# Kernel optimization log

Hardware: AMD Instinct MI355X
Metric: run time of the kernel (lower is better)

The kernel has to match this reference:

```python
import jax, jax.numpy as jnp
import numpy as np
import math

EPS = 1.1920929e-07  # torch.finfo(float32).eps, used by nn.RMSNorm when eps=None
N_HEADS = 16

def _rmsnorm(x, w):
    return x * jax.lax.rsqrt(jnp.mean(x * x, axis=-1, keepdims=True) + EPS) * w

def setup_inputs() -> dict:
    key = jax.random.key(0)
    D, V, FF = 1024, 32000, 2048
    NS, IPS = 4, 8
    B, T = 2, 1024
    ks = jax.random.split(key, 8)
    sd = 0.02
    g = lambda i, shape: jax.random.normal(ks[i], shape, jnp.float32) * sd
    return {
        "tokens": jax.random.randint(ks[0], (B, T), 0, V),
        "embed_w": g(1, (V, D)),
        "qkv_w": g(2, (3 * D, D)),
        "o_w": g(3, (D, D)),
        "gate_w": g(4, (FF, D)),
        "up_w": g(5, (FF, D)),
        "down_w": g(6, (D, FF)),
        "norm1_w": jnp.ones((D,), jnp.float32),
        "norm2_w": jnp.ones((D,), jnp.float32),
        "scale_gamma": jnp.ones((NS, D), jnp.float32),
        "scale_beta": jnp.zeros((NS, D), jnp.float32),
        "iter_scale": jnp.ones((NS, IPS), jnp.float32),
        "norm_w": jnp.ones((D,), jnp.float32),
        "lm_head_w": g(7, (V, D)),
    }

def _block(x, gamma, beta, qkv_w, o_w, gate_w, up_w, down_w, norm1_w, norm2_w):
    B, T, D = x.shape
    hd = D // N_HEADS
    # pre-attn norm + FiLM modulation
    h = _rmsnorm(x, norm1_w) * gamma + beta
    qkv = (h @ qkv_w.T).reshape(B, T, 3, N_HEADS, hd)
    q = jnp.transpose(qkv[:, :, 0], (0, 2, 1, 3))  # [B,H,T,hd]
    k = jnp.transpose(qkv[:, :, 1], (0, 2, 1, 3))
    v = jnp.transpose(qkv[:, :, 2], (0, 2, 1, 3))
    scores = jnp.einsum('bhqd,bhkd->bhqk', q, k) / math.sqrt(hd)
    causal = jnp.tril(jnp.ones((T, T), dtype=bool))
    scores = jnp.where(causal, scores, -jnp.inf)
    attn = jax.nn.softmax(scores, axis=-1)
    out = jnp.einsum('bhqk,bhkd->bhqd', attn, v)
    out = jnp.transpose(out, (0, 2, 1, 3)).reshape(B, T, D)
    x = x + out @ o_w.T
    # pre-FFN norm + FiLM modulation, SwiGLU
    h2 = _rmsnorm(x, norm2_w) * gamma + beta
    x = x + (jax.nn.silu(h2 @ gate_w.T) * (h2 @ up_w.T)) @ down_w.T
    return x

def reference(tokens, embed_w, qkv_w, o_w, gate_w, up_w, down_w, norm1_w,
              norm2_w, scale_gamma, scale_beta, iter_scale, norm_w, lm_head_w):
    NS, IPS = iter_scale.shape
    x = embed_w[tokens].astype(jnp.float32)  # [B,T,D]
    # flatten (scale, iter) schedule to per-virtual-layer params [NS*IPS, ...]
    gammas = jnp.repeat(scale_gamma, IPS, axis=0)
    betas = jnp.repeat(scale_beta, IPS, axis=0)
    iters = iter_scale.reshape(-1)

    @jax.checkpoint
    def step(x, per):
        g, b, s = per
        y = _block(x, g, b, qkv_w, o_w, gate_w, up_w, down_w, norm1_w, norm2_w)
        return x + (y - x) * s, None

    x, _ = jax.lax.scan(step, x, (gammas, betas, iters))
    return _rmsnorm(x, norm_w) @ lm_head_w.T  # [B,T,V]
```

## Files before the change

kernel.cpp:

```cpp
#include <hip/hip_runtime.h>

typedef __bf16 bf16;
typedef __attribute__((ext_vector_type(8))) __bf16 bf16x8;
typedef __attribute__((ext_vector_type(4))) __bf16 bf16x4;
typedef __attribute__((ext_vector_type(4))) float f32x4;

#define MFMA16(a,b,c) __builtin_amdgcn_mfma_f32_16x16x32_bf16((a),(b),(c),0,0,0)

__device__ __forceinline__ void gload16(const void* g, void* l) {
    __builtin_amdgcn_global_load_lds((const __attribute__((address_space(1))) void*)g,
                                     (__attribute__((address_space(3))) void*)l, 16, 0, 0);
}

__device__ __forceinline__ int xcd_swizzle(int orig, int nwg) {
    int q = nwg >> 3, r = nwg & 7;
    int xcd = orig & 7, loc = orig >> 3;
    int base = (xcd < r) ? xcd * (q + 1) : r * (q + 1) + (xcd - r) * q;
    return base + loc;
}


__global__ __launch_bounds__(256) void cvt_kernel(const float* __restrict__ in,
                                                  bf16* __restrict__ out, int n4) {
    int stride = gridDim.x * 256;
    for (int i = blockIdx.x * 256 + threadIdx.x; i < n4; i += stride) {
        float4 v = ((const float4*)in)[i];
        bf16x4 o;
        o[0] = (bf16)v.x; o[1] = (bf16)v.y; o[2] = (bf16)v.z; o[3] = (bf16)v.w;
        ((bf16x4*)out)[i] = o;
    }
}

__global__ __launch_bounds__(256) void embed_kernel(const int* __restrict__ tok,
                                                    const float* __restrict__ ew,
                                                    float* __restrict__ X) {
    int m = blockIdx.x;
    int t = tok[m];
    ((float4*)(X + (size_t)m * 1024))[threadIdx.x] =
        ((const float4*)(ew + (size_t)t * 1024))[threadIdx.x];
}

template <bool FILM>
__global__ __launch_bounds__(256) void rmsnorm_kernel(const float* __restrict__ X,
                                                      const float* __restrict__ w,
                                                      const float* __restrict__ gamma,
                                                      const float* __restrict__ beta,
                                                      bf16* __restrict__ H) {
    int m = blockIdx.x, t = threadIdx.x;
    float4 xv = ((const float4*)(X + (size_t)m * 1024))[t];
    float ss = xv.x * xv.x + xv.y * xv.y + xv.z * xv.z + xv.w * xv.w;
#pragma unroll
    for (int off = 1; off < 64; off <<= 1) ss += __shfl_xor(ss, off);
    __shared__ float red[4];
    if ((t & 63) == 0) red[t >> 6] = ss;
    __syncthreads();
    float tot = red[0] + red[1] + red[2] + red[3];
    float sc = rsqrtf(tot * (1.0f / 1024.0f) + 1.1920929e-07f);
    float4 wv = ((const float4*)w)[t];
    float r0 = xv.x * sc * wv.x, r1 = xv.y * sc * wv.y;
    float r2 = xv.z * sc * wv.z, r3 = xv.w * sc * wv.w;
    if (FILM) {
        float4 gv = ((const float4*)gamma)[t];
        float4 bv = ((const float4*)beta)[t];
        r0 = r0 * gv.x + bv.x; r1 = r1 * gv.y + bv.y;
        r2 = r2 * gv.z + bv.z; r3 = r3 * gv.w + bv.w;
    }
    bf16x4 o;
    o[0] = (bf16)r0; o[1] = (bf16)r1; o[2] = (bf16)r2; o[3] = (bf16)r3;
    ((bf16x4*)(H + (size_t)m * 1024))[t] = o;
}


template <int MT, int MODE, bool BNF>
__device__ __forceinline__ void gemm_body(const bf16* __restrict__ A,
                                          const bf16* __restrict__ B,
                                          int GN, int GM, int N, int K,
                                          bf16* __restrict__ Cb, float* __restrict__ Cf,
                                          const float* __restrict__ Xin,
                                          const float* __restrict__ Xin2,
                                          float* __restrict__ Xout,
                                          const float* __restrict__ sptr,
                                          bf16* __restrict__ VTp) {
    constexpr int BM = 32 * MT;
    __shared__ __align__(16) bf16 As[BM * 64];
    __shared__ __align__(16) bf16 Bs[128 * 64];
    const int wg = xcd_swizzle(blockIdx.x, GN * GM);
    int bn, bm;
    if (BNF) { bm = wg / GN; bn = wg - bm * GN; }
    else     { bn = wg / GM; bm = wg - bn * GM; }
    const int tid = threadIdx.x, lane = tid & 63, w = tid >> 6;
    const int wr = w >> 1, wc = w & 1, lr = lane & 15, lg = lane >> 4;
    const bf16* Ab = A + (size_t)bm * BM * K;
    const bf16* Bb = B + (size_t)bn * 128 * K;

    f32x4 acc[MT][4];
#pragma unroll
    for (int i = 0; i < MT; ++i)
#pragma unroll
        for (int j = 0; j < 4; ++j) acc[i][j] = (f32x4){0.f, 0.f, 0.f, 0.f};

    for (int kt = 0; kt < K; kt += 64) {
        __syncthreads();
#pragma unroll
        for (int i = 0; i < MT; ++i) {
            int cw = i * 256 + w * 64;
            int cid = cw + lane;
            gload16(Ab + (size_t)(cid >> 3) * K + kt + (cid & 7) * 8, As + cw * 8);
        }
#pragma unroll
        for (int i = 0; i < 4; ++i) {
            int cw = i * 256 + w * 64;
            int cid = cw + lane;
            gload16(Bb + (size_t)(cid >> 3) * K + kt + (cid & 7) * 8, Bs + cw * 8);
        }
        __syncthreads();
#pragma unroll
        for (int kk = 0; kk < 64; kk += 32) {
            bf16x8 af[MT], bfr[4];
#pragma unroll
            for (int mi = 0; mi < MT; ++mi)
                af[mi] = *(const bf16x8*)(As + (wr * (16 * MT) + mi * 16 + lr) * 64 + kk + lg * 8);
#pragma unroll
            for (int ni = 0; ni < 4; ++ni)
                bfr[ni] = *(const bf16x8*)(Bs + (wc * 64 + ni * 16 + lr) * 64 + kk + lg * 8);
#pragma unroll
            for (int mi = 0; mi < MT; ++mi)
#pragma unroll
                for (int ni = 0; ni < 4; ++ni)
                    acc[mi][ni] = MFMA16(af[mi], bfr[ni], acc[mi][ni]);
        }
    }

    float s1 = (MODE == 2) ? sptr[0] : 0.f;
    if (MODE == 4 && bn >= 16) {
#pragma unroll
        for (int mi = 0; mi < MT; ++mi) {
#pragma unroll
            for (int ni = 0; ni < 4; ++ni) {
                int row0 = bm * BM + wr * (16 * MT) + mi * 16 + lg * 4;
                int col = bn * 128 + wc * 64 + ni * 16 + lr;
                int h = (col - 2048) >> 6, d = (col - 2048) & 63;
                int bb = row0 >> 10, t0 = row0 & 1023;
                bf16x4 pv;
#pragma unroll
                for (int j = 0; j < 4; ++j) pv[j] = (bf16)acc[mi][ni][j];
                *(bf16x4*)(VTp + (size_t)(bb * 16 + h) * 65536 + (size_t)d * 1024 + t0) = pv;
            }
        }
        return;
    }
#pragma unroll
    for (int mi = 0; mi < MT; ++mi) {
#pragma unroll
        for (int ni = 0; ni < 4; ++ni) {
#pragma unroll
            for (int j = 0; j < 4; ++j) {
                int row = bm * BM + wr * (16 * MT) + mi * 16 + lg * 4 + j;
                int col = bn * 128 + wc * 64 + ni * 16 + lr;
                size_t idx = (size_t)row * N + col;
                float v = acc[mi][ni][j];
                if (MODE == 0 || MODE == 4) Cb[idx] = (bf16)v;
                else if (MODE == 1) Xout[idx] = Xin[idx] + v;
                else if (MODE == 2) Xout[idx] = Xin[idx] + s1 * (Xin2[idx] - Xin[idx] + v);
                else Cf[idx] = v;
            }
        }
    }
}

__global__ __launch_bounds__(256, 4) void gemm_qkv(const bf16* A, const bf16* B, int GN, int GM,
                                                   int N, int K, bf16* Cb, bf16* VTp) {
    gemm_body<2, 4, false>(A, B, GN, GM, N, K, Cb, nullptr, nullptr, nullptr, nullptr, nullptr, VTp);
}
__global__ __launch_bounds__(256, 4) void gemm_oproj(const bf16* A, const bf16* B, int GN, int GM,
                                                     int N, int K, const float* Xin, float* Xout) {
    gemm_body<1, 1, true>(A, B, GN, GM, N, K, nullptr, nullptr, Xin, nullptr, Xout, nullptr, nullptr);
}
__global__ __launch_bounds__(256, 4) void gemm_down(const bf16* A, const bf16* B, int GN, int GM,
                                                    int N, int K, const float* Xin, const float* Xin2,
                                                    float* Xout, const float* sptr) {
    gemm_body<1, 2, true>(A, B, GN, GM, N, K, nullptr, nullptr, Xin, Xin2, Xout, sptr, nullptr);
}
__global__ __launch_bounds__(256, 4) void gemm_lmhead(const bf16* A, const bf16* B, int GN, int GM,
                                                      int N, int K, float* Cf) {
    gemm_body<4, 3, false>(A, B, GN, GM, N, K, nullptr, Cf, nullptr, nullptr, nullptr, nullptr, nullptr);
}


__global__ __launch_bounds__(256, 4) void gemm_gateup(const bf16* __restrict__ A,
                                                      const bf16* __restrict__ Bg,
                                                      const bf16* __restrict__ Bu,
                                                      bf16* __restrict__ FF) {
    const int K = 1024, N = 2048;
    __shared__ __align__(16) bf16 As[64 * 64];
    __shared__ __align__(16) bf16 Gs[128 * 64];
    __shared__ __align__(16) bf16 Us[128 * 64];
    const int wg = xcd_swizzle(blockIdx.x, 512);
    const int bn = wg >> 5, bm = wg & 31;
    const int tid = threadIdx.x, lane = tid & 63, w = tid >> 6;
    const int wr = w >> 1, wc = w & 1, lr = lane & 15, lg = lane >> 4;
    const bf16* Ab = A + (size_t)bm * 64 * K;
    const bf16* Gb = Bg + (size_t)bn * 128 * K;
    const bf16* Ub = Bu + (size_t)bn * 128 * K;

    f32x4 ag[2][4], au[2][4];
#pragma unroll
    for (int i = 0; i < 2; ++i)
#pragma unroll
        for (int j = 0; j < 4; ++j) {
            ag[i][j] = (f32x4){0.f, 0.f, 0.f, 0.f};
            au[i][j] = (f32x4){0.f, 0.f, 0.f, 0.f};
        }

    for (int kt = 0; kt < K; kt += 64) {
        __syncthreads();
#pragma unroll
        for (int i = 0; i < 2; ++i) {
            int cw = i * 256 + w * 64;
            int cid = cw + lane;
            gload16(Ab + (size_t)(cid >> 3) * K + kt + (cid & 7) * 8, As + cw * 8);
        }
#pragma unroll
        for (int i = 0; i < 4; ++i) {
            int cw = i * 256 + w * 64;
            int cid = cw + lane;
            size_t ro = (size_t)(cid >> 3) * K + kt + (cid & 7) * 8;
            gload16(Gb + ro, Gs + cw * 8);
            gload16(Ub + ro, Us + cw * 8);
        }
        __syncthreads();
#pragma unroll
        for (int kk = 0; kk < 64; kk += 32) {
            bf16x8 af[2], gf[4], uf[4];
#pragma unroll
            for (int mi = 0; mi < 2; ++mi)
                af[mi] = *(const bf16x8*)(As + (wr * 32 + mi * 16 + lr) * 64 + kk + lg * 8);
#pragma unroll
            for (int ni = 0; ni < 4; ++ni) {
                gf[ni] = *(const bf16x8*)(Gs + (wc * 64 + ni * 16 + lr) * 64 + kk + lg * 8);
                uf[ni] = *(const bf16x8*)(Us + (wc * 64 + ni * 16 + lr) * 64 + kk + lg * 8);
            }
#pragma unroll
            for (int mi = 0; mi < 2; ++mi)
#pragma unroll
                for (int ni = 0; ni < 4; ++ni) {
                    ag[mi][ni] = MFMA16(af[mi], gf[ni], ag[mi][ni]);
                    au[mi][ni] = MFMA16(af[mi], uf[ni], au[mi][ni]);
                }
        }
    }

#pragma unroll
    for (int mi = 0; mi < 2; ++mi) {
#pragma unroll
        for (int ni = 0; ni < 4; ++ni) {
#pragma unroll
            for (int j = 0; j < 4; ++j) {
                int row = bm * 64 + wr * 32 + mi * 16 + lg * 4 + j;
                int col = bn * 128 + wc * 64 + ni * 16 + lr;
                float g = ag[mi][ni][j], u = au[mi][ni][j];
                float sg = g / (1.0f + __expf(-g));
                FF[(size_t)row * N + col] = (bf16)(sg * u);
            }
        }
    }
}


__global__ __launch_bounds__(256) void attn_kernel(const bf16* __restrict__ QKV,
                                                   const bf16* __restrict__ VTg,
                                                   bf16* __restrict__ AO) {
    const int qt = (blockIdx.x & 1) ? (15 - (blockIdx.x >> 1)) : (blockIdx.x >> 1);
    const int bh = blockIdx.y;
    const int b = bh >> 4, h = bh & 15;
    const int tid = threadIdx.x;
    const int w = tid >> 6, lane = tid & 63;
    const int lr = lane & 15, lg = lane >> 4;

    __shared__ __align__(16) bf16 Ks[64 * 72];
    __shared__ __align__(16) bf16 Vt[64 * 72];
    __shared__ __align__(16) bf16 Ps[4 * 16 * 72];
    bf16* Pw = Ps + w * 16 * 72;

    const int qrow = b * 1024 + qt * 64 + w * 16 + lr;
    const bf16* qptr = QKV + (size_t)qrow * 3072 + h * 64;
    const bf16* vt_src = VTg + (size_t)bh * 65536;
    bf16x8 qf0 = *(const bf16x8*)(qptr + lg * 8);
    bf16x8 qf1 = *(const bf16x8*)(qptr + 32 + lg * 8);

    f32x4 o[4];
#pragma unroll
    for (int i = 0; i < 4; ++i) o[i] = (f32x4){0.f, 0.f, 0.f, 0.f};
    float m_run = -1e30f, l_run = 0.f;
    const int gq = qt * 64 + w * 16 + lr;

    for (int kt = 0; kt <= qt; ++kt) {
        __syncthreads();
#pragma unroll
        for (int i = 0; i < 2; ++i) {
            int cid = tid + 256 * i;
            int r = cid >> 3, c8 = (cid & 7) * 8;
            const bf16* kvrow = QKV + (size_t)(b * 1024 + kt * 64 + r) * 3072 + h * 64;
            *(bf16x8*)(Ks + r * 72 + c8) = *(const bf16x8*)(kvrow + 1024 + c8);
            *(bf16x8*)(Vt + r * 72 + c8) =
                *(const bf16x8*)(vt_src + (size_t)r * 1024 + kt * 64 + c8);
        }
        __syncthreads();

        f32x4 st[4];
#pragma unroll
        for (int i = 0; i < 4; ++i) st[i] = (f32x4){0.f, 0.f, 0.f, 0.f};
        __builtin_amdgcn_s_setprio(1);
#pragma unroll
        for (int ki = 0; ki < 4; ++ki) {
            bf16x8 kf0 = *(const bf16x8*)(Ks + (ki * 16 + lr) * 72 + lg * 8);
            bf16x8 kf1 = *(const bf16x8*)(Ks + (ki * 16 + lr) * 72 + 32 + lg * 8);
            st[ki] = MFMA16(kf0, qf0, st[ki]);
            st[ki] = MFMA16(kf1, qf1, st[ki]);
        }
        __builtin_amdgcn_s_setprio(0);
        bool diag = (kt == qt);
        float pm = -1e30f;
#pragma unroll
        for (int ki = 0; ki < 4; ++ki) {
#pragma unroll
            for (int j = 0; j < 4; ++j) {
                float sv = st[ki][j] * 0.125f;
                if (diag) {
                    int gk = kt * 64 + ki * 16 + lg * 4 + j;
                    if (gk > gq) sv = -1e30f;
                }
                st[ki][j] = sv;
                pm = fmaxf(pm, sv);
            }
        }
        pm = fmaxf(pm, __shfl_xor(pm, 16));
        pm = fmaxf(pm, __shfl_xor(pm, 32));
        float m_new = fmaxf(m_run, pm);
        float alpha = __expf(m_run - m_new);
        float rs = 0.f;
#pragma unroll
        for (int ki = 0; ki < 4; ++ki) {
            bf16x4 pb;
#pragma unroll
            for (int j = 0; j < 4; ++j) {
                float pv = __expf(st[ki][j] - m_new);
                rs += pv;
                pb[j] = (bf16)pv;
            }
            *(bf16x4*)(Pw + lr * 72 + ki * 16 + lg * 4) = pb;
        }
        rs += __shfl_xor(rs, 16);
        rs += __shfl_xor(rs, 32);
        l_run = l_run * alpha + rs;
        m_run = m_new;
#pragma unroll
        for (int di = 0; di < 4; ++di) o[di] *= alpha;
        __builtin_amdgcn_s_setprio(1);
#pragma unroll
        for (int dk = 0; dk < 2; ++dk) {
            bf16x8 pf = *(const bf16x8*)(Pw + lr * 72 + dk * 32 + lg * 8);
#pragma unroll
            for (int di = 0; di < 4; ++di) {
                bf16x8 vf = *(const bf16x8*)(Vt + (di * 16 + lr) * 72 + dk * 32 + lg * 8);
                o[di] = MFMA16(vf, pf, o[di]);
            }
        }
        __builtin_amdgcn_s_setprio(0);
    }
    float inv = 1.0f / l_run;
    bf16* optr = AO + (size_t)qrow * 1024 + h * 64;
#pragma unroll
    for (int di = 0; di < 4; ++di) {
        bf16x4 ov;
#pragma unroll
        for (int j = 0; j < 4; ++j) ov[j] = (bf16)(o[di][j] * inv);
        *(bf16x4*)(optr + di * 16 + lg * 4) = ov;
    }
}


extern "C" void kernel_launch(void* const* d_in, const int* in_sizes, int n_in,
                              void* d_out, int out_size, void* d_ws, size_t ws_size,
                              hipStream_t stream) {
    const int* tokens = (const int*)d_in[0];
    const float* embed_w = (const float*)d_in[1];
    const float* qkv_w = (const float*)d_in[2];
    const float* o_w = (const float*)d_in[3];
    const float* gate_w = (const float*)d_in[4];
    const float* up_w = (const float*)d_in[5];
    const float* down_w = (const float*)d_in[6];
    const float* norm1_w = (const float*)d_in[7];
    const float* norm2_w = (const float*)d_in[8];
    const float* scale_gamma = (const float*)d_in[9];
    const float* scale_beta = (const float*)d_in[10];
    const float* iter_scale = (const float*)d_in[11];
    const float* norm_w = (const float*)d_in[12];
    const float* lm_head_w = (const float*)d_in[13];

    char* p = (char*)d_ws;
    auto alloc = [&](size_t nbytes) -> char* {
        char* r = p;
        p += (nbytes + 255) & ~(size_t)255;
        return r;
    };
    bf16* WQKV = (bf16*)alloc(3072ull * 1024 * 2);
    bf16* WO   = (bf16*)alloc(1024ull * 1024 * 2);
    bf16* WG   = (bf16*)alloc(2048ull * 1024 * 2);
    bf16* WU   = (bf16*)alloc(2048ull * 1024 * 2);
    bf16* WD   = (bf16*)alloc(1024ull * 2048 * 2);
    bf16* WLM  = (bf16*)alloc(32000ull * 1024 * 2);
    float* X   = (float*)alloc(2048ull * 1024 * 4);
    float* X1  = (float*)alloc(2048ull * 1024 * 4);
    bf16* H    = (bf16*)alloc(2048ull * 1024 * 2);
    bf16* QKVb = (bf16*)alloc(2048ull * 3072 * 2);
    bf16* VT   = (bf16*)alloc(2048ull * 1024 * 2);
    bf16* AO   = (bf16*)alloc(2048ull * 1024 * 2);
    bf16* FF   = (bf16*)alloc(2048ull * 2048 * 2);

    cvt_kernel<<<1024, 256, 0, stream>>>(qkv_w, WQKV, 3072 * 1024 / 4);
    cvt_kernel<<<1024, 256, 0, stream>>>(o_w, WO, 1024 * 1024 / 4);
    cvt_kernel<<<1024, 256, 0, stream>>>(gate_w, WG, 2048 * 1024 / 4);
    cvt_kernel<<<1024, 256, 0, stream>>>(up_w, WU, 2048 * 1024 / 4);
    cvt_kernel<<<1024, 256, 0, stream>>>(down_w, WD, 1024 * 2048 / 4);
    cvt_kernel<<<2048, 256, 0, stream>>>(lm_head_w, WLM, 32000 * 1024 / 4);
    embed_kernel<<<2048, 256, 0, stream>>>(tokens, embed_w, X);

    for (int l = 0; l < 32; ++l) {
        const float* gm = scale_gamma + (size_t)(l >> 3) * 1024;
        const float* bt = scale_beta + (size_t)(l >> 3) * 1024;
        rmsnorm_kernel<true><<<2048, 256, 0, stream>>>(X, norm1_w, gm, bt, H);
        gemm_qkv<<<24 * 32, 256, 0, stream>>>(H, WQKV, 24, 32, 3072, 1024, QKVb, VT);
        attn_kernel<<<dim3(16, 32), 256, 0, stream>>>(QKVb, VT, AO);
        gemm_oproj<<<8 * 64, 256, 0, stream>>>(AO, WO, 8, 64, 1024, 1024, X, X1);
        rmsnorm_kernel<true><<<2048, 256, 0, stream>>>(X1, norm2_w, gm, bt, H);
        gemm_gateup<<<512, 256, 0, stream>>>(H, WG, WU, FF);
        gemm_down<<<8 * 64, 256, 0, stream>>>(FF, WD, 8, 64, 1024, 2048, X, X1, X, iter_scale + l);
    }
    rmsnorm_kernel<false><<<2048, 256, 0, stream>>>(X, norm_w, nullptr, nullptr, H);
    gemm_lmhead<<<250 * 16, 256, 0, stream>>>(H, WLM, 250, 16, 32000, 1024, (float*)d_out);
}
```

Measured before the change: 4.605 ms.

## Fuse RMSNorm+FiLM into GEMM A-staging using epilogue-computed row sum-of-squares

Removes the two per-layer RMSNorm kernels. The o-proj and down GEMM epilogues now write per-column-tile partial sums of squares of the residual, and the QKV and gate/up GEMMs finish the reduction, then normalize, scale and convert fp32 X to bf16 while staging the A tile. Norm weight times gamma is precomputed per scale. This saves launches and the H write/read round trip. In exchange, A staging becomes synchronous fp32 loads with conversion instead of async global-to-LDS copies, and each X tile is re-read and renormalized by every column block.

```diff
diff --git a/kernel.cpp b/kernel.cpp
--- a/kernel.cpp
+++ b/kernel.cpp
@@ -6,6 +6,7 @@
 typedef __attribute__((ext_vector_type(4))) float f32x4;
 
 #define MFMA16(a,b,c) __builtin_amdgcn_mfma_f32_16x16x32_bf16((a),(b),(c),0,0,0)
+#define RMS_EPS 1.1920929e-07f
 
 __device__ __forceinline__ void gload16(const void* g, void* l) {
     __builtin_amdgcn_global_load_lds((const __attribute__((address_space(1))) void*)g,
@@ -31,56 +32,93 @@
     }
 }
 
+__global__ __launch_bounds__(256) void wg_kernel(const float* __restrict__ norm1_w,
+                                                 const float* __restrict__ norm2_w,
+                                                 const float* __restrict__ scale_gamma,
+                                                 float* __restrict__ WG1,
+                                                 float* __restrict__ WG2) {
+    int b = blockIdx.x;
+    int s = b >> 1, which = b & 1;
+    int c = threadIdx.x * 4;
+    float4 g = *(const float4*)(scale_gamma + s * 1024 + c);
+    const float* w = which ? norm2_w : norm1_w;
+    float* dst = which ? WG2 : WG1;
+    float4 wv = *(const float4*)(w + c);
+    float4 o = {wv.x * g.x, wv.y * g.y, wv.z * g.z, wv.w * g.w};
+    *(float4*)(dst + s * 1024 + c) = o;
+}
+
 __global__ __launch_bounds__(256) void embed_kernel(const int* __restrict__ tok,
                                                     const float* __restrict__ ew,
-                                                    float* __restrict__ X) {
-    int m = blockIdx.x;
-    int t = tok[m];
-    ((float4*)(X + (size_t)m * 1024))[threadIdx.x] =
-        ((const float4*)(ew + (size_t)t * 1024))[threadIdx.x];
-}
-
-template <bool FILM>
-__global__ __launch_bounds__(256) void rmsnorm_kernel(const float* __restrict__ X,
-                                                      const float* __restrict__ w,
-                                                      const float* __restrict__ gamma,
-                                                      const float* __restrict__ beta,
-                                                      bf16* __restrict__ H) {
+                                                    float* __restrict__ X,
+                                                    float* __restrict__ SQ0) {
     int m = blockIdx.x, t = threadIdx.x;
-    float4 xv = ((const float4*)(X + (size_t)m * 1024))[t];
-    float ss = xv.x * xv.x + xv.y * xv.y + xv.z * xv.z + xv.w * xv.w;
+    int tk = tok[m];
+    float4 v = ((const float4*)(ew + (size_t)tk * 1024))[t];
+    ((float4*)(X + (size_t)m * 1024))[t] = v;
+    float ss = v.x * v.x + v.y * v.y + v.z * v.z + v.w * v.w;
 #pragma unroll
     for (int off = 1; off < 64; off <<= 1) ss += __shfl_xor(ss, off);
     __shared__ float red[4];
     if ((t & 63) == 0) red[t >> 6] = ss;
     __syncthreads();
     float tot = red[0] + red[1] + red[2] + red[3];
-    float sc = rsqrtf(tot * (1.0f / 1024.0f) + 1.1920929e-07f);
+    if (t < 8) SQ0[t * 2048 + m] = (t == 0) ? tot : 0.f;
+}
+
+__global__ __launch_bounds__(256) void rmsnorm_kernel(const float* __restrict__ X,
+                                                      const float* __restrict__ w,
+                                                      bf16* __restrict__ H) {
+    int m = blockIdx.x, t = threadIdx.x;
+    float4 xv = ((const float4*)(X + (size_t)m * 1024))[t];
+    float ss = xv.x * xv.x + xv.y * xv.y + xv.z * xv.z + xv.w * xv.w;
+#pragma unroll
+    for (int off = 1; off < 64; off <<= 1) ss += __shfl_xor(ss, off);
+    __shared__ float red[4];
+    if ((t & 63) == 0) red[t >> 6] = ss;
+    __syncthreads();
+    float tot = red[0] + red[1] + red[2] + red[3];
+    float sc = rsqrtf(tot * (1.0f / 1024.0f) + RMS_EPS);
     float4 wv = ((const float4*)w)[t];
-    float r0 = xv.x * sc * wv.x, r1 = xv.y * sc * wv.y;
-    float r2 = xv.z * sc * wv.z, r3 = xv.w * sc * wv.w;
-    if (FILM) {
-        float4 gv = ((const float4*)gamma)[t];
-        float4 bv = ((const float4*)beta)[t];
-        r0 = r0 * gv.x + bv.x; r1 = r1 * gv.y + bv.y;
-        r2 = r2 * gv.z + bv.z; r3 = r3 * gv.w + bv.w;
-    }
     bf16x4 o;
-    o[0] = (bf16)r0; o[1] = (bf16)r1; o[2] = (bf16)r2; o[3] = (bf16)r3;
+    o[0] = (bf16)(xv.x * sc * wv.x); o[1] = (bf16)(xv.y * sc * wv.y);
+    o[2] = (bf16)(xv.z * sc * wv.z); o[3] = (bf16)(xv.w * sc * wv.w);
     ((bf16x4*)(H + (size_t)m * 1024))[t] = o;
 }
 
+template <int NCH>
+__device__ __forceinline__ void stage_a_norm(const float* __restrict__ Xs, int row0, int kt,
+                                             const float* __restrict__ WG,
+                                             const float* __restrict__ BT,
+                                             const float* __restrict__ srms,
+                                             bf16* __restrict__ As, int tid) {
+#pragma unroll
+    for (int i = 0; i < NCH; ++i) {
+        int cid = i * 256 + tid;
+        int r = cid >> 3, c8 = (cid & 7) * 8;
+        const float* xp = Xs + (size_t)(row0 + r) * 1024 + kt + c8;
+        float4 xa = *(const float4*)xp, xb = *(const float4*)(xp + 4);
+        float4 wa = *(const float4*)(WG + kt + c8), wb = *(const float4*)(WG + kt + c8 + 4);
+        float4 ba = *(const float4*)(BT + kt + c8), bb = *(const float4*)(BT + kt + c8 + 4);
+        float sc = srms[r];
+        bf16x8 hv;
+        hv[0] = (bf16)(xa.x * sc * wa.x + ba.x);
+        hv[1] = (bf16)(xa.y * sc * wa.y + ba.y);
+        hv[2] = (bf16)(xa.z * sc * wa.z + ba.z);
+        hv[3] = (bf16)(xa.w * sc * wa.w + ba.w);
+        hv[4] = (bf16)(xb.x * sc * wb.x + bb.x);
+        hv[5] = (bf16)(xb.y * sc * wb.y + bb.y);
+        hv[6] = (bf16)(xb.z * sc * wb.z + bb.z);
+        hv[7] = (bf16)(xb.w * sc * wb.w + bb.w);
+        *(bf16x8*)(As + cid * 8) = hv;
+    }
+}
 
 template <int MT, int MODE, bool BNF>
 __device__ __forceinline__ void gemm_body(const bf16* __restrict__ A,
                                           const bf16* __restrict__ B,
                                           int GN, int GM, int N, int K,
-                                          bf16* __restrict__ Cb, float* __restrict__ Cf,
-                                          const float* __restrict__ Xin,
-                                          const float* __restrict__ Xin2,
-                                          float* __restrict__ Xout,
-                                          const float* __restrict__ sptr,
-                                          bf16* __restrict__ VTp) {
+                                          bf16* __restrict__ Cb, float* __restrict__ Cf) {
     constexpr int BM = 32 * MT;
     __shared__ __align__(16) bf16 As[BM * 64];
     __shared__ __align__(16) bf16 Bs[128 * 64];
@@ -131,24 +169,6 @@
         }
     }
 
-    float s1 = (MODE == 2) ? sptr[0] : 0.f;
-    if (MODE == 4 && bn >= 16) {
-#pragma unroll
-        for (int mi = 0; mi < MT; ++mi) {
-#pragma unroll
-            for (int ni = 0; ni < 4; ++ni) {
-                int row0 = bm * BM + wr * (16 * MT) + mi * 16 + lg * 4;
-                int col = bn * 128 + wc * 64 + ni * 16 + lr;
-                int h = (col - 2048) >> 6, d = (col - 2048) & 63;
-                int bb = row0 >> 10, t0 = row0 & 1023;
-                bf16x4 pv;
-#pragma unroll
-                for (int j = 0; j < 4; ++j) pv[j] = (bf16)acc[mi][ni][j];
-                *(bf16x4*)(VTp + (size_t)(bb * 16 + h) * 65536 + (size_t)d * 1024 + t0) = pv;
-            }
-        }
-        return;
-    }
 #pragma unroll
     for (int mi = 0; mi < MT; ++mi) {
 #pragma unroll
@@ -158,36 +178,199 @@
                 int row = bm * BM + wr * (16 * MT) + mi * 16 + lg * 4 + j;
                 int col = bn * 128 + wc * 64 + ni * 16 + lr;
                 size_t idx = (size_t)row * N + col;
-                float v = acc[mi][ni][j];
-                if (MODE == 0 || MODE == 4) Cb[idx] = (bf16)v;
-                else if (MODE == 1) Xout[idx] = Xin[idx] + v;
-                else if (MODE == 2) Xout[idx] = Xin[idx] + s1 * (Xin2[idx] - Xin[idx] + v);
-                else Cf[idx] = v;
-            }
-        }
-    }
-}
-
-__global__ __launch_bounds__(256, 4) void gemm_qkv(const bf16* A, const bf16* B, int GN, int GM,
-                                                   int N, int K, bf16* Cb, bf16* VTp) {
-    gemm_body<2, 4, false>(A, B, GN, GM, N, K, Cb, nullptr, nullptr, nullptr, nullptr, nullptr, VTp);
-}
+                if (MODE == 0) Cb[idx] = (bf16)acc[mi][ni][j];
+                else Cf[idx] = acc[mi][ni][j];
+            }
+        }
+    }
+}
+
+__global__ __launch_bounds__(256, 4) void gemm_lmhead(const bf16* A, const bf16* B, int GN, int GM,
+                                                      int N, int K, float* Cf) {
+    gemm_body<4, 3, false>(A, B, GN, GM, N, K, nullptr, Cf);
+}
+
+__global__ __launch_bounds__(256, 4) void gemm_qkv(const float* __restrict__ X,
+                                                   const float* __restrict__ SQ0,
+                                                   const float* __restrict__ WG,
+                                                   const float* __restrict__ BT,
+                                                   const bf16* __restrict__ B,
+                                                   bf16* __restrict__ Cb,
+                                                   bf16* __restrict__ VTp) {
+    const int GN = 24, GM = 32, N = 3072, K = 1024;
+    __shared__ __align__(16) bf16 As[64 * 64];
+    __shared__ __align__(16) bf16 Bs[128 * 64];
+    __shared__ float srms[64];
+    const int wg = xcd_swizzle(blockIdx.x, GN * GM);
+    const int bn = wg / GM, bm = wg - bn * GM;
+    const int tid = threadIdx.x, lane = tid & 63, w = tid >> 6;
+    const int wr = w >> 1, wc = w & 1, lr = lane & 15, lg = lane >> 4;
+    const int row0 = bm * 64;
+    const bf16* Bb = B + (size_t)bn * 128 * K;
+
+    if (tid < 64) {
+        float s = 0.f;
+#pragma unroll
+        for (int k = 0; k < 8; ++k) s += SQ0[k * 2048 + row0 + tid];
+        srms[tid] = rsqrtf(s * (1.0f / 1024.0f) + RMS_EPS);
+    }
+
+    f32x4 acc[2][4];
+#pragma unroll
+    for (int i = 0; i < 2; ++i)
+#pragma unroll
+        for (int j = 0; j < 4; ++j) acc[i][j] = (f32x4){0.f, 0.f, 0.f, 0.f};
+
+    for (int kt = 0; kt < K; kt += 64) {
+        __syncthreads();
+        stage_a_norm<2>(X, row0, kt, WG, BT, srms, As, tid);
+#pragma unroll
+        for (int i = 0; i < 4; ++i) {
+            int cw = i * 256 + w * 64;
+            int cid = cw + lane;
+            gload16(Bb + (size_t)(cid >> 3) * K + kt + (cid & 7) * 8, Bs + cw * 8);
+        }
+        __syncthreads();
+#pragma unroll
+        for (int kk = 0; kk < 64; kk += 32) {
+            bf16x8 af[2], bfr[4];
+#pragma unroll
+            for (int mi = 0; mi < 2; ++mi)
+                af[mi] = *(const bf16x8*)(As + (wr * 32 + mi * 16 + lr) * 64 + kk + lg * 8);
+#pragma unroll
+            for (int ni = 0; ni < 4; ++ni)
+                bfr[ni] = *(const bf16x8*)(Bs + (wc * 64 + ni * 16 + lr) * 64 + kk + lg * 8);
+#pragma unroll
+            for (int mi = 0; mi < 2; ++mi)
+#pragma unroll
+                for (int ni = 0; ni < 4; ++ni)
+                    acc[mi][ni] = MFMA16(af[mi], bfr[ni], acc[mi][ni]);
+        }
+    }
+
+    if (bn >= 16) {
+#pragma unroll
+        for (int mi = 0; mi < 2; ++mi) {
+#pragma unroll
+            for (int ni = 0; ni < 4; ++ni) {
+                int r0 = row0 + wr * 32 + mi * 16 + lg * 4;
+                int col = bn * 128 + wc * 64 + ni * 16 + lr;
+                int h = (col - 2048) >> 6, d = (col - 2048) & 63;
+                int bb = r0 >> 10, t0 = r0 & 1023;
+                bf16x4 pv;
+#pragma unroll
+                for (int j = 0; j < 4; ++j) pv[j] = (bf16)acc[mi][ni][j];
+                *(bf16x4*)(VTp + (size_t)(bb * 16 + h) * 65536 + (size_t)d * 1024 + t0) = pv;
+            }
+        }
+        return;
+    }
+#pragma unroll
+    for (int mi = 0; mi < 2; ++mi) {
+#pragma unroll
+        for (int ni = 0; ni < 4; ++ni) {
+#pragma unroll
+            for (int j = 0; j < 4; ++j) {
+                int row = row0 + wr * 32 + mi * 16 + lg * 4 + j;
+                int col = bn * 128 + wc * 64 + ni * 16 + lr;
+                Cb[(size_t)row * 3072 + col] = (bf16)acc[mi][ni][j];
+            }
+        }
+    }
+}
+
+template <int MODE>
+__device__ __forceinline__ void gemm_resid_body(const bf16* __restrict__ A,
+                                                const bf16* __restrict__ B,
+                                                int GN, int GM, int N, int K,
+                                                const float* __restrict__ Xin,
+                                                const float* __restrict__ Xin2,
+                                                float* __restrict__ Xout,
+                                                const float* __restrict__ sptr,
+                                                float* __restrict__ SQout) {
+    __shared__ __align__(16) bf16 As[32 * 64];
+    __shared__ __align__(16) bf16 Bs[128 * 64];
+    __shared__ float part[32][2];
+    const int wg = xcd_swizzle(blockIdx.x, GN * GM);
+    const int bm = wg / GN, bn = wg - bm * GN;
+    const int tid = threadIdx.x, lane = tid & 63, w = tid >> 6;
+    const int wr = w >> 1, wc = w & 1, lr = lane & 15, lg = lane >> 4;
+    const bf16* Ab = A + (size_t)bm * 32 * K;
+    const bf16* Bb = B + (size_t)bn * 128 * K;
+
+    f32x4 acc[4];
+#pragma unroll
+    for (int j = 0; j < 4; ++j) acc[j] = (f32x4){0.f, 0.f, 0.f, 0.f};
+
+    for (int kt = 0; kt < K; kt += 64) {
+        __syncthreads();
+        {
+            int cid = tid;
+            int cw = w * 64;
+            gload16(Ab + (size_t)(cid >> 3) * K + kt + (cid & 7) * 8, As + cw * 8);
+        }
+#pragma unroll
+        for (int i = 0; i < 4; ++i) {
+            int cw = i * 256 + w * 64;
+            int cid = cw + lane;
+            gload16(Bb + (size_t)(cid >> 3) * K + kt + (cid & 7) * 8, Bs + cw * 8);
+        }
+        __syncthreads();
+#pragma unroll
+        for (int kk = 0; kk < 64; kk += 32) {
+            bf16x8 af = *(const bf16x8*)(As + (wr * 16 + lr) * 64 + kk + lg * 8);
+            bf16x8 bfr[4];
+#pragma unroll
+            for (int ni = 0; ni < 4; ++ni)
+                bfr[ni] = *(const bf16x8*)(Bs + (wc * 64 + ni * 16 + lr) * 64 + kk + lg * 8);
+#pragma unroll
+            for (int ni = 0; ni < 4; ++ni)
+                acc[ni] = MFMA16(af, bfr[ni], acc[ni]);
+        }
+    }
+
+    float s1 = (MODE == 2) ? sptr[0] : 0.f;
+    __syncthreads();
+#pragma unroll
+    for (int j = 0; j < 4; ++j) {
+        int row = bm * 32 + wr * 16 + lg * 4 + j;
+        float sj = 0.f;
+#pragma unroll
+        for (int ni = 0; ni < 4; ++ni) {
+            int col = bn * 128 + wc * 64 + ni * 16 + lr;
+            size_t idx = (size_t)row * N + col;
+            float v = acc[ni][j];
+            float ov;
+            if (MODE == 1) ov = Xin[idx] + v;
+            else           ov = Xin[idx] + s1 * (Xin2[idx] - Xin[idx] + v);
+            Xout[idx] = ov;
+            sj += ov * ov;
+        }
+        sj += __shfl_xor(sj, 1);
+        sj += __shfl_xor(sj, 2);
+        sj += __shfl_xor(sj, 4);
+        sj += __shfl_xor(sj, 8);
+        if (lr == 0) part[wr * 16 + lg * 4 + j][wc] = sj;
+    }
+    __syncthreads();
+    if (tid < 32) SQout[bn * 2048 + bm * 32 + tid] = part[tid][0] + part[tid][1];
+}
+
 __global__ __launch_bounds__(256, 4) void gemm_oproj(const bf16* A, const bf16* B, int GN, int GM,
-                                                     int N, int K, const float* Xin, float* Xout) {
-    gemm_body<1, 1, true>(A, B, GN, GM, N, K, nullptr, nullptr, Xin, nullptr, Xout, nullptr, nullptr);
+                                                     int N, int K, const float* Xin, float* Xout,
+                                                     float* SQout) {
+    gemm_resid_body<1>(A, B, GN, GM, N, K, Xin, nullptr, Xout, nullptr, SQout);
 }
 __global__ __launch_bounds__(256, 4) void gemm_down(const bf16* A, const bf16* B, int GN, int GM,
                                                     int N, int K, const float* Xin, const float* Xin2,
-                                                    float* Xout, const float* sptr) {
-    gemm_body<1, 2, true>(A, B, GN, GM, N, K, nullptr, nullptr, Xin, Xin2, Xout, sptr, nullptr);
-}
-__global__ __launch_bounds__(256, 4) void gemm_lmhead(const bf16* A, const bf16* B, int GN, int GM,
-                                                      int N, int K, float* Cf) {
-    gemm_body<4, 3, false>(A, B, GN, GM, N, K, nullptr, Cf, nullptr, nullptr, nullptr, nullptr, nullptr);
-}
-
-
-__global__ __launch_bounds__(256, 4) void gemm_gateup(const bf16* __restrict__ A,
+                                                    float* Xout, const float* sptr, float* SQout) {
+    gemm_resid_body<2>(A, B, GN, GM, N, K, Xin, Xin2, Xout, sptr, SQout);
+}
+
+__global__ __launch_bounds__(256, 4) void gemm_gateup(const float* __restrict__ X1,
+                                                      const float* __restrict__ SQ1,
+                                                      const float* __restrict__ WG,
+                                                      const float* __restrict__ BT,
                                                       const bf16* __restrict__ Bg,
                                                       const bf16* __restrict__ Bu,
                                                       bf16* __restrict__ FF) {
@@ -195,13 +378,21 @@
     __shared__ __align__(16) bf16 As[64 * 64];
     __shared__ __align__(16) bf16 Gs[128 * 64];
     __shared__ __align__(16) bf16 Us[128 * 64];
+    __shared__ float srms[64];
     const int wg = xcd_swizzle(blockIdx.x, 512);
     const int bn = wg >> 5, bm = wg & 31;
     const int tid = threadIdx.x, lane = tid & 63, w = tid >> 6;
     const int wr = w >> 1, wc = w & 1, lr = lane & 15, lg = lane >> 4;
-    const bf16* Ab = A + (size_t)bm * 64 * K;
+    const int row0 = bm * 64;
     const bf16* Gb = Bg + (size_t)bn * 128 * K;
     const bf16* Ub = Bu + (size_t)bn * 128 * K;
+
+    if (tid < 64) {
+        float s = 0.f;
+#pragma unroll
+        for (int k = 0; k < 8; ++k) s += SQ1[k * 2048 + row0 + tid];
+        srms[tid] = rsqrtf(s * (1.0f / 1024.0f) + RMS_EPS);
+    }
 
     f32x4 ag[2][4], au[2][4];
 #pragma unroll
@@ -214,12 +405,7 @@
 
     for (int kt = 0; kt < K; kt += 64) {
         __syncthreads();
-#pragma unroll
-        for (int i = 0; i < 2; ++i) {
-            int cw = i * 256 + w * 64;
-            int cid = cw + lane;
-            gload16(Ab + (size_t)(cid >> 3) * K + kt + (cid & 7) * 8, As + cw * 8);
-        }
+        stage_a_norm<2>(X1, row0, kt, WG, BT, srms, As, tid);
 #pragma unroll
         for (int i = 0; i < 4; ++i) {
             int cw = i * 256 + w * 64;
@@ -256,7 +442,7 @@
         for (int ni = 0; ni < 4; ++ni) {
 #pragma unroll
             for (int j = 0; j < 4; ++j) {
-                int row = bm * 64 + wr * 32 + mi * 16 + lg * 4 + j;
+                int row = row0 + wr * 32 + mi * 16 + lg * 4 + j;
                 int col = bn * 128 + wc * 64 + ni * 16 + lr;
                 float g = ag[mi][ni][j], u = au[mi][ni][j];
                 float sg = g / (1.0f + __expf(-g));
@@ -417,6 +603,10 @@
     bf16* VT   = (bf16*)alloc(2048ull * 1024 * 2);
     bf16* AO   = (bf16*)alloc(2048ull * 1024 * 2);
     bf16* FF   = (bf16*)alloc(2048ull * 2048 * 2);
+    float* SQ0 = (float*)alloc(8ull * 2048 * 4);
+    float* SQ1 = (float*)alloc(8ull * 2048 * 4);
+    float* WG1 = (float*)alloc(4ull * 1024 * 4);
+    float* WG2 = (float*)alloc(4ull * 1024 * 4);
 
     cvt_kernel<<<1024, 256, 0, stream>>>(qkv_w, WQKV, 3072 * 1024 / 4);
     cvt_kernel<<<1024, 256, 0, stream>>>(o_w, WO, 1024 * 1024 / 4);
@@ -424,19 +614,19 @@
     cvt_kernel<<<1024, 256, 0, stream>>>(up_w, WU, 2048 * 1024 / 4);
     cvt_kernel<<<1024, 256, 0, stream>>>(down_w, WD, 1024 * 2048 / 4);
     cvt_kernel<<<2048, 256, 0, stream>>>(lm_head_w, WLM, 32000 * 1024 / 4);
-    embed_kernel<<<2048, 256, 0, stream>>>(tokens, embed_w, X);
+    wg_kernel<<<8, 256, 0, stream>>>(norm1_w, norm2_w, scale_gamma, WG1, WG2);
+    embed_kernel<<<2048, 256, 0, stream>>>(tokens, embed_w, X, SQ0);
 
     for (int l = 0; l < 32; ++l) {
-        const float* gm = scale_gamma + (size_t)(l >> 3) * 1024;
-        const float* bt = scale_beta + (size_t)(l >> 3) * 1024;
-        rmsnorm_kernel<true><<<2048, 256, 0, stream>>>(X, norm1_w, gm, bt, H);
-        gemm_qkv<<<24 * 32, 256, 0, stream>>>(H, WQKV, 24, 32, 3072, 1024, QKVb, VT);
+        int s = l >> 3;
+        const float* bt = scale_beta + (size_t)s * 1024;
+        gemm_qkv<<<24 * 32, 256, 0, stream>>>(X, SQ0, WG1 + s * 1024, bt, WQKV, QKVb, VT);
         attn_kernel<<<dim3(16, 32), 256, 0, stream>>>(QKVb, VT, AO);
-        gemm_oproj<<<8 * 64, 256, 0, stream>>>(AO, WO, 8, 64, 1024, 1024, X, X1);
-        rmsnorm_kernel<true><<<2048, 256, 0, stream>>>(X1, norm2_w, gm, bt, H);
-        gemm_gateup<<<512, 256, 0, stream>>>(H, WG, WU, FF);
-        gemm_down<<<8 * 64, 256, 0, stream>>>(FF, WD, 8, 64, 1024, 2048, X, X1, X, iter_scale + l);
-    }
-    rmsnorm_kernel<false><<<2048, 256, 0, stream>>>(X, norm_w, nullptr, nullptr, H);
+        gemm_oproj<<<8 * 64, 256, 0, stream>>>(AO, WO, 8, 64, 1024, 1024, X, X1, SQ1);
+        gemm_gateup<<<512, 256, 0, stream>>>(X1, SQ1, WG2 + s * 1024, bt, WG, WU, FF);
+        gemm_down<<<8 * 64, 256, 0, stream>>>(FF, WD, 8, 64, 1024, 2048, X, X1, X,
+                                              iter_scale + l, SQ0);
+    }
+    rmsnorm_kernel<<<2048, 256, 0, stream>>>(X, norm_w, H);
     gemm_lmhead<<<250 * 16, 256, 0, stream>>>(H, WLM, 250, 16, 32000, 1024, (float*)d_out);
 }
```

Result: slower. 5.130 ms (+11.4%).
